# Kernel optimization log

Measured on AMD Instinct MI355X. Metric: run time of the kernel, lower is better.

## Reference

```python
import jax, jax.numpy as jnp
import numpy as np

N = 50000          # nodes
E = 800000         # edges (before self-loops)
F_IN, F_HID, F_OUT = 128, 64, 64
NEG_SLOPE_ATT = 0.2   # GATConv internal leaky_relu
NEG_SLOPE_ACT = 0.01  # F.leaky_relu default between layers


def setup_inputs() -> dict:
    key = jax.random.key(0)
    ks = jax.random.split(key, 16)

    def glorot(k, shape):
        fan = float(sum(shape)) if len(shape) > 1 else float(shape[0])
        return jax.random.normal(k, shape, jnp.float32) * (2.0 / fan) ** 0.5

    return {
        "x": jax.random.normal(ks[0], (N, F_IN), jnp.float32),
        "edge_index": jax.random.randint(ks[1], (2, E), 0, N, dtype=jnp.int64),
        "W1": glorot(ks[2], (F_IN, F_HID)),
        "a_src1": glorot(ks[3], (F_HID,)),
        "a_dst1": glorot(ks[4], (F_HID,)),
        "b1": jnp.zeros((F_HID,), jnp.float32),
        "W2": glorot(ks[5], (F_HID, F_HID)),
        "a_src2": glorot(ks[6], (F_HID,)),
        "a_dst2": glorot(ks[7], (F_HID,)),
        "b2": jnp.zeros((F_HID,), jnp.float32),
        "W3": glorot(ks[8], (F_HID, F_OUT)),
        "a_src3": glorot(ks[9], (F_OUT,)),
        "a_dst3": glorot(ks[10], (F_OUT,)),
        "b3": jnp.zeros((F_OUT,), jnp.float32),
    }


def gat_conv(h, src, dst, W, a_src, a_dst, b):
    # Single-head PyG GATConv: project, per-edge scores, segment softmax over dst, scatter-add.
    z = h @ W                              # [N, C]
    e_src = z @ a_src                      # [N]
    e_dst = z @ a_dst                      # [N]
    e = jax.nn.leaky_relu(e_src[src] + e_dst[dst], NEG_SLOPE_ATT)  # [E']
    m = jax.ops.segment_max(e, dst, num_segments=N)
    ex = jnp.exp(e - m[dst])
    denom = jax.ops.segment_sum(ex, dst, num_segments=N)
    alpha = ex / (denom[dst] + 1e-16)      # segment softmax (PyG adds 1e-16)
    out = jax.ops.segment_sum(alpha[:, None] * z[src], dst, num_segments=N) + b
    return out, alpha


def reference(x, edge_index, W1, a_src1, a_dst1, b1, W2, a_src2, a_dst2, b2, W3, a_src3, a_dst3, b3):
    # add_self_loops=True (GATConv default): append (i, i) for every node
    loops = jnp.arange(N, dtype=edge_index.dtype)
    ei = jnp.concatenate([edge_index, jnp.stack([loops, loops])], axis=1)  # [2, E+N]
    src, dst = ei[0], ei[1]

    h = x
    alpha = None
    for (W, asr, ads, b) in ((W1, a_src1, a_dst1, b1),
                             (W2, a_src2, a_dst2, b2),
                             (W3, a_src3, a_dst3, b3)):
        h, alpha = gat_conv(h, src, dst, W, asr, ads, b)
        h = jax.nn.leaky_relu(h, NEG_SLOPE_ACT)
    return (h, ei, alpha)
```

## Files before the change

### kernel.cpp

```cpp
#include <hip/hip_runtime.h>
#include <hip/hip_bf16.h>
#include <hip/hip_fp8.h>

#define NN 50000
#define EE 800000
#define E2 850000
#define F_IN 128
#define F_HID 64
#define NCHUNK ((NN + 255) / 256)
#define NTILE  ((NN + 63) / 64)
#define AGGB 2048

#define PNB 32
#define BCAP 32768
#define CBCH 512
#define CBB ((EE + CBCH - 1) / CBCH)
#define CBCAP 48
#define SLICEB 64

__device__ __forceinline__ unsigned char f32_to_fp8(float x) {
    __hip_fp8_e4m3 t(x);
    return t.__x;
}
__device__ __forceinline__ float fp8_to_f32(unsigned char b) {
    __hip_fp8_e4m3 t; t.__x = b;
    return (float)t;
}

#if defined(__has_builtin)
#  if __has_builtin(__builtin_amdgcn_cvt_f32_fp8)
#    define CVT_FP8(v, s) __builtin_amdgcn_cvt_f32_fp8((v), (s))
#  endif
#endif
#ifndef CVT_FP8
#  define CVT_FP8(v, s) fp8_to_f32(((v) >> (8 * (s))) & 255)
#endif

__global__ __launch_bounds__(256) void cast_bin_kernel(const int* __restrict__ ei,
                                                       int* __restrict__ bin_cur,
                                                       unsigned long long* __restrict__ bins,
                                                       float* __restrict__ ei_out) {
    __shared__ unsigned long long buf[PNB * CBCAP];
    __shared__ int cnt[PNB];
    __shared__ int gbase[PNB];
    __shared__ int pfx[PNB + 1];
    int tid = threadIdx.x;
    if (tid < PNB) cnt[tid] = 0;
    __syncthreads();

    int e0 = blockIdx.x * CBCH;
    int e1 = e0 + CBCH; if (e1 > EE) e1 = EE;
    for (int e = e0 + tid; e < e1; e += 256) {
        int s = ei[e], d = ei[EE + e];
        ei_out[e]      = (float)s;
        ei_out[E2 + e] = (float)d;
        int b = (int)(((long long)d * PNB) / NN);
        unsigned long long pk = ((unsigned long long)(unsigned)d << 32) | (unsigned)s;
        int r = atomicAdd(&cnt[b], 1);
        if (r < CBCAP) buf[b * CBCAP + r] = pk;
        else {
            int p = atomicAdd(&bin_cur[b], 1);
            if (p < BCAP) bins[(size_t)b * BCAP + p] = pk;
        }
    }
    __syncthreads();
    if (tid < PNB) {
        int c = cnt[tid]; if (c > CBCAP) c = CBCAP;
        cnt[tid] = c;
        gbase[tid] = c ? atomicAdd(&bin_cur[tid], c) : 0;
    }
    __syncthreads();
    if (tid == 0) {
        int run = 0;
        for (int b = 0; b < PNB; ++b) { pfx[b] = run; run += cnt[b]; }
        pfx[PNB] = run;
    }
    __syncthreads();
    int total = pfx[PNB];
    for (int idx = tid; idx < total; idx += 256) {
        int lo = 0, hi = PNB;
        while (hi - lo > 1) { int mid = (lo + hi) >> 1; if (pfx[mid] <= idx) lo = mid; else hi = mid; }
        int b = lo, li = idx - pfx[b];
        int p = gbase[b] + li;
        if (p < BCAP) bins[(size_t)b * BCAP + p] = buf[b * CBCAP + li];
    }
}

__global__ __launch_bounds__(256) void count_bins(const int* __restrict__ bin_cur,
                                                  const unsigned long long* __restrict__ bins,
                                                  int* __restrict__ deg) {
    int b = blockIdx.x & (PNB - 1);
    int slice = blockIdx.x >> 5;
    int cnt = bin_cur[b];
    if (cnt > BCAP) cnt = BCAP;
    const unsigned long long* bp = bins + (size_t)b * BCAP;
    for (int i = slice * 256 + threadIdx.x; i < cnt; i += SLICEB * 256) {
        int d = (int)(bp[i] >> 32);
        atomicAdd(&deg[d], 1);
    }
}

__global__ __launch_bounds__(256) void scan_part12(const int* __restrict__ deg,
                                                   int* __restrict__ csum,
                                                   int* __restrict__ ticket) {
    int i = blockIdx.x * 256 + threadIdx.x;
    int v = (i < NN) ? deg[i] + 1 : 0;
#pragma unroll
    for (int d = 32; d; d >>= 1) v += __shfl_xor(v, d);
    __shared__ int ws[4];
    if ((threadIdx.x & 63) == 0) ws[threadIdx.x >> 6] = v;
    __syncthreads();
    __shared__ int isLast;
    if (threadIdx.x == 0) {
        atomicExch(&csum[blockIdx.x], ws[0] + ws[1] + ws[2] + ws[3]);
        __threadfence();
        isLast = (atomicAdd(ticket, 1) == gridDim.x - 1) ? 1 : 0;
    }
    __syncthreads();
    if (isLast) {
        __threadfence();
        __shared__ int sd[256];
        int t = threadIdx.x;
        int v2 = (t < NCHUNK) ? atomicAdd(&csum[t], 0) : 0;
        sd[t] = v2;
        __syncthreads();
        for (int off = 1; off < 256; off <<= 1) {
            int o = (t >= off) ? sd[t - off] : 0;
            __syncthreads();
            sd[t] += o;
            __syncthreads();
        }
        if (t < NCHUNK) atomicExch(&csum[t], sd[t] - v2);
    }
}

__global__ __launch_bounds__(256) void scan_part3(const int* __restrict__ deg,
                                                  const int* __restrict__ csum,
                                                  int* __restrict__ offs,
                                                  int* __restrict__ cursor,
                                                  int* __restrict__ src_sorted,
                                                  float* __restrict__ ei_out) {
    __shared__ int sd[256];
    int t = threadIdx.x;
    int i = blockIdx.x * 256 + t;
    int v = (i < NN) ? deg[i] + 1 : 0;
    sd[t] = v;
    __syncthreads();
    for (int off = 1; off < 256; off <<= 1) {
        int o = (t >= off) ? sd[t - off] : 0;
        __syncthreads();
        sd[t] += o;
        __syncthreads();
    }
    if (i < NN) {
        int ex = sd[t] - v + csum[blockIdx.x];
        offs[i] = ex;
        cursor[i] = ex + 1;
        src_sorted[ex] = i;
        ei_out[EE + i]      = (float)i;
        ei_out[E2 + EE + i] = (float)i;
    }
}

__global__ __launch_bounds__(256) void scatter_bins(const int* __restrict__ bin_cur,
                                                    const unsigned long long* __restrict__ bins,
                                                    int* __restrict__ cursor,
                                                    int* __restrict__ src_sorted) {
    int b = blockIdx.x & (PNB - 1);
    int slice = blockIdx.x >> 5;
    int cnt = bin_cur[b];
    if (cnt > BCAP) cnt = BCAP;
    const unsigned long long* bp = bins + (size_t)b * BCAP;
    for (int i = slice * 256 + threadIdx.x; i < cnt; i += SLICEB * 256) {
        unsigned long long v = bp[i];
        int d = (int)(v >> 32);
        int s = (int)(v & 0xffffffffu);
        int pos = atomicAdd(&cursor[d], 1);
        src_sorted[pos] = s;
    }
}

template <int K>
__global__ __launch_bounds__(256) void gemm_tile(const float* __restrict__ h,
                                                 const float* __restrict__ W,
                                                 const float* __restrict__ a_src,
                                                 const float* __restrict__ a_dst,
                                                 unsigned char* __restrict__ z8,
                                                 float* __restrict__ es,
                                                 float* __restrict__ ed) {
    constexpr int LDA = K + 4;
    __shared__ float Alds[64 * LDA];
    __shared__ float Blds[K * 64];

    int tid = threadIdx.x;
    int base = blockIdx.x * 64;

    {
        constexpr int F4R = K / 4;
        for (int t = tid; t < 64 * F4R; t += 256) {
            int r = t / F4R;
            int c4 = t % F4R;
            int gr = base + r;
            if (gr >= NN) gr = NN - 1;
            float4 v = *(const float4*)(h + (size_t)gr * K + c4 * 4);
            *(float4*)(&Alds[r * LDA + c4 * 4]) = v;
        }
    }
    for (int t = tid; t < K * 16; t += 256) {
        float4 v = *(const float4*)(W + t * 4);
        *(float4*)(&Blds[t * 4]) = v;
    }
    __syncthreads();

    int tx = tid & 15;
    int ty = tid >> 4;

    float acc[4][4] = {};
#pragma unroll 4
    for (int k = 0; k < K; k += 4) {
        float4 a[4], b[4];
#pragma unroll
        for (int i = 0; i < 4; ++i)
            a[i] = *(const float4*)(&Alds[(4 * ty + i) * LDA + k]);
#pragma unroll
        for (int kk = 0; kk < 4; ++kk)
            b[kk] = *(const float4*)(&Blds[(k + kk) * 64 + 4 * tx]);
#pragma unroll
        for (int i = 0; i < 4; ++i) {
            acc[i][0] = fmaf(a[i].x, b[0].x, acc[i][0]);
            acc[i][1] = fmaf(a[i].x, b[0].y, acc[i][1]);
            acc[i][2] = fmaf(a[i].x, b[0].z, acc[i][2]);
            acc[i][3] = fmaf(a[i].x, b[0].w, acc[i][3]);
            acc[i][0] = fmaf(a[i].y, b[1].x, acc[i][0]);
            acc[i][1] = fmaf(a[i].y, b[1].y, acc[i][1]);
            acc[i][2] = fmaf(a[i].y, b[1].z, acc[i][2]);
            acc[i][3] = fmaf(a[i].y, b[1].w, acc[i][3]);
            acc[i][0] = fmaf(a[i].z, b[2].x, acc[i][0]);
            acc[i][1] = fmaf(a[i].z, b[2].y, acc[i][1]);
            acc[i][2] = fmaf(a[i].z, b[2].z, acc[i][2]);
            acc[i][3] = fmaf(a[i].z, b[2].w, acc[i][3]);
            acc[i][0] = fmaf(a[i].w, b[3].x, acc[i][0]);
            acc[i][1] = fmaf(a[i].w, b[3].y, acc[i][1]);
            acc[i][2] = fmaf(a[i].w, b[3].z, acc[i][2]);
            acc[i][3] = fmaf(a[i].w, b[3].w, acc[i][3]);
        }
    }

    float4 as4 = *(const float4*)(a_src + 4 * tx);
    float4 ad4 = *(const float4*)(a_dst + 4 * tx);
    float ps[4], pd[4];
#pragma unroll
    for (int i = 0; i < 4; ++i) {
        int gr = base + 4 * ty + i;
        if (gr < NN) {
            unsigned int pk = (unsigned int)f32_to_fp8(acc[i][0])
                            | ((unsigned int)f32_to_fp8(acc[i][1]) << 8)
                            | ((unsigned int)f32_to_fp8(acc[i][2]) << 16)
                            | ((unsigned int)f32_to_fp8(acc[i][3]) << 24);
            *(unsigned int*)(&z8[(size_t)gr * 64 + 4 * tx]) = pk;
        }
        ps[i] = acc[i][0] * as4.x + acc[i][1] * as4.y + acc[i][2] * as4.z + acc[i][3] * as4.w;
        pd[i] = acc[i][0] * ad4.x + acc[i][1] * ad4.y + acc[i][2] * ad4.z + acc[i][3] * ad4.w;
    }
#pragma unroll
    for (int d = 1; d < 16; d <<= 1) {
#pragma unroll
        for (int i = 0; i < 4; ++i) {
            ps[i] += __shfl_xor(ps[i], d);
            pd[i] += __shfl_xor(pd[i], d);
        }
    }
    if (tx == 0) {
#pragma unroll
        for (int i = 0; i < 4; ++i) {
            int gr = base + 4 * ty + i;
            if (gr < NN) { es[gr] = ps[i]; ed[gr] = pd[i]; }
        }
    }
}

__global__ __launch_bounds__(256) void aggregate(const int* __restrict__ offs,
                                                 const int* __restrict__ deg,
                                                 const int* __restrict__ src_sorted,
                                                 const float* __restrict__ es,
                                                 const float* __restrict__ ed,
                                                 const unsigned char* __restrict__ z8,
                                                 const float* __restrict__ bias,
                                                 float* __restrict__ hout,
                                                 float* __restrict__ denom_out) {
    int tid = threadIdx.x;
    int lane = tid & 63;
    int wave = blockIdx.x * 4 + (tid >> 6);
    const int NW = AGGB * 4;

    int sub  = lane >> 4;
    int fgrp = (lane & 15) * 4;
    const unsigned char* zp = z8 + fgrp;
    float4 bi4 = *(const float4*)(bias + fgrp);

    int n = wave;
    if (n >= NN) return;
    n = __builtin_amdgcn_readfirstlane(n);
    int off = offs[n];
    int dg = deg[n] + 1;
    float edn = ed[n];
    int sv = src_sorted[off + ((lane < dg) ? lane : 0)];
    float ese = es[sv];

    while (true) {
        int n2 = n + NW;
        bool more = (n2 < NN);
        int off2 = 0, dg2 = 0; float edn2 = 0.f;
        if (more) {
            n2 = __builtin_amdgcn_readfirstlane(n2);
            off2 = offs[n2]; dg2 = deg[n2] + 1; edn2 = ed[n2];
        }

        float dsum = 0.f;
        float a0 = 0.f, a1 = 0.f, a2 = 0.f, a3 = 0.f;
        for (int b0 = 0; b0 < dg; b0 += 64) {
            int bl = dg - b0; if (bl > 64) bl = 64;
            int svb; float esv;
            if (b0 == 0) { svb = sv; esv = ese; }
            else {
                svb = src_sorted[off + b0 + ((lane < bl) ? lane : 0)];
                esv = es[svb];
            }
            float e = esv + edn;
            e = (e > 0.f) ? e : 0.2f * e;
            float w = (lane < bl) ? __expf(e) : 0.f;
            dsum += w;

            int ng = (bl + 3) >> 2;
            int j = 0;
            for (; j + 4 <= ng; j += 4) {
                int i0 = 4 * j + sub;
                int   s0 = __shfl(svb, i0);
                int   s1 = __shfl(svb, i0 + 4);
                int   s2 = __shfl(svb, i0 + 8);
                int   s3 = __shfl(svb, i0 + 12);
                unsigned int v0 = *(const unsigned int*)(zp + (size_t)s0 * 64);
                unsigned int v1 = *(const unsigned int*)(zp + (size_t)s1 * 64);
                unsigned int v2 = *(const unsigned int*)(zp + (size_t)s2 * 64);
                unsigned int v3 = *(const unsigned int*)(zp + (size_t)s3 * 64);
                float w0 = __shfl(w, i0);
                float w1 = __shfl(w, i0 + 4);
                float w2 = __shfl(w, i0 + 8);
                float w3 = __shfl(w, i0 + 12);
                a0 = fmaf(w0, CVT_FP8(v0, 0), a0);
                a1 = fmaf(w0, CVT_FP8(v0, 1), a1);
                a2 = fmaf(w0, CVT_FP8(v0, 2), a2);
                a3 = fmaf(w0, CVT_FP8(v0, 3), a3);
                a0 = fmaf(w1, CVT_FP8(v1, 0), a0);
                a1 = fmaf(w1, CVT_FP8(v1, 1), a1);
                a2 = fmaf(w1, CVT_FP8(v1, 2), a2);
                a3 = fmaf(w1, CVT_FP8(v1, 3), a3);
                a0 = fmaf(w2, CVT_FP8(v2, 0), a0);
                a1 = fmaf(w2, CVT_FP8(v2, 1), a1);
                a2 = fmaf(w2, CVT_FP8(v2, 2), a2);
                a3 = fmaf(w2, CVT_FP8(v2, 3), a3);
                a0 = fmaf(w3, CVT_FP8(v3, 0), a0);
                a1 = fmaf(w3, CVT_FP8(v3, 1), a1);
                a2 = fmaf(w3, CVT_FP8(v3, 2), a2);
                a3 = fmaf(w3, CVT_FP8(v3, 3), a3);
            }
            for (; j < ng; ++j) {
                int i0 = 4 * j + sub;
                int   s0 = __shfl(svb, i0);
                unsigned int v0 = *(const unsigned int*)(zp + (size_t)s0 * 64);
                float w0 = __shfl(w, i0);
                a0 = fmaf(w0, CVT_FP8(v0, 0), a0);
                a1 = fmaf(w0, CVT_FP8(v0, 1), a1);
                a2 = fmaf(w0, CVT_FP8(v0, 2), a2);
                a3 = fmaf(w0, CVT_FP8(v0, 3), a3);
            }
        }

        int sv2 = 0;
        if (more) sv2 = src_sorted[off2 + ((lane < dg2) ? lane : 0)];

        a0 += __shfl_xor(a0, 16); a1 += __shfl_xor(a1, 16);
        a2 += __shfl_xor(a2, 16); a3 += __shfl_xor(a3, 16);
        a0 += __shfl_xor(a0, 32); a1 += __shfl_xor(a1, 32);
        a2 += __shfl_xor(a2, 32); a3 += __shfl_xor(a3, 32);
#pragma unroll
        for (int d = 32; d; d >>= 1) dsum += __shfl_xor(dsum, d);

        float ese2 = 0.f;
        if (more) ese2 = es[sv2];

        float inv = 1.f / (dsum + 1e-16f);
        if (lane < 16) {
            float4 o;
            o.x = a0 * inv + bi4.x;
            o.y = a1 * inv + bi4.y;
            o.z = a2 * inv + bi4.z;
            o.w = a3 * inv + bi4.w;
            o.x = (o.x > 0.f) ? o.x : 0.01f * o.x;
            o.y = (o.y > 0.f) ? o.y : 0.01f * o.y;
            o.z = (o.z > 0.f) ? o.z : 0.01f * o.z;
            o.w = (o.w > 0.f) ? o.w : 0.01f * o.w;
            *(float4*)(hout + (size_t)n * 64 + fgrp) = o;
        }
        if (lane == 0) denom_out[n] = dsum;

        if (!more) break;
        n = n2; off = off2; dg = dg2; edn = edn2; sv = sv2; ese = ese2;
    }
}

__global__ __launch_bounds__(256) void alpha_kernel(const int* __restrict__ ei,
                                                    const float* __restrict__ es,
                                                    const float* __restrict__ ed,
                                                    const float* __restrict__ denom,
                                                    float* __restrict__ alpha_out) {
    int e = blockIdx.x * 256 + threadIdx.x;
    if (e >= E2) return;
    int s, d;
    if (e < EE) { s = ei[e]; d = ei[EE + e]; }
    else        { s = d = e - EE; }
    float x = es[s] + ed[d];
    x = (x > 0.f) ? x : 0.2f * x;
    alpha_out[e] = __expf(x) / (denom[d] + 1e-16f);
}

extern "C" void kernel_launch(void* const* d_in, const int* in_sizes, int n_in,
                              void* d_out, int out_size, void* d_ws, size_t ws_size,
                              hipStream_t stream) {
    const float* x   = (const float*)d_in[0];
    const int*   ei  = (const int*)d_in[1];
    const float* W1  = (const float*)d_in[2];
    const float* as1 = (const float*)d_in[3];
    const float* ad1 = (const float*)d_in[4];
    const float* b1  = (const float*)d_in[5];
    const float* W2  = (const float*)d_in[6];
    const float* as2 = (const float*)d_in[7];
    const float* ad2 = (const float*)d_in[8];
    const float* b2  = (const float*)d_in[9];
    const float* W3  = (const float*)d_in[10];
    const float* as3 = (const float*)d_in[11];
    const float* ad3 = (const float*)d_in[12];
    const float* b3  = (const float*)d_in[13];

    float* out       = (float*)d_out;
    float* h_out     = out;
    float* ei_out    = out + (size_t)NN * 64;
    float* alpha_out = ei_out + 2 * (size_t)E2;

    char* w = (char*)d_ws;
    auto carve = [&](size_t bytes) {
        void* p = (void*)w;
        w += (bytes + 255) & ~size_t(255);
        return p;
    };
    float* h1  = (float*)carve((size_t)NN * 64 * 4);
    float* h2  = (float*)carve((size_t)NN * 64 * 4);
    unsigned char* z8 = (unsigned char*)carve((size_t)NN * 64);
    float* es  = (float*)carve((size_t)NN * 4);
    float* ed  = (float*)carve((size_t)NN * 4);
    float* denom = (float*)carve((size_t)NN * 4);
    int* deg        = (int*)carve(((size_t)NN + 64) * 4);
    int* ticket     = deg + NN;
    int* bin_cur    = deg + NN + 1;
    int* offs       = (int*)carve((size_t)NN * 4);
    int* cursor     = (int*)carve((size_t)NN * 4);
    int* csum       = (int*)carve((size_t)NCHUNK * 4);
    int* src_sorted = (int*)carve((size_t)E2 * 4);
    unsigned long long* bins = (unsigned long long*)carve((size_t)PNB * BCAP * 8);

    const int EB = (E2 + 255) / 256;

    hipMemsetAsync(deg, 0, ((size_t)NN + 64) * 4, stream);
    cast_bin_kernel<<<CBB, 256, 0, stream>>>(ei, bin_cur, bins, ei_out);
    count_bins<<<PNB * SLICEB, 256, 0, stream>>>(bin_cur, bins, deg);
    scan_part12<<<NCHUNK, 256, 0, stream>>>(deg, csum, ticket);
    scan_part3<<<NCHUNK, 256, 0, stream>>>(deg, csum, offs, cursor, src_sorted, ei_out);
    scatter_bins<<<PNB * SLICEB, 256, 0, stream>>>(bin_cur, bins, cursor, src_sorted);

    gemm_tile<F_IN><<<NTILE, 256, 0, stream>>>(x, W1, as1, ad1, z8, es, ed);
    aggregate<<<AGGB, 256, 0, stream>>>(offs, deg, src_sorted, es, ed, z8, b1, h1, denom);
    gemm_tile<F_HID><<<NTILE, 256, 0, stream>>>(h1, W2, as2, ad2, z8, es, ed);
    aggregate<<<AGGB, 256, 0, stream>>>(offs, deg, src_sorted, es, ed, z8, b2, h2, denom);
    gemm_tile<F_HID><<<NTILE, 256, 0, stream>>>(h2, W3, as3, ad3, z8, es, ed);
    aggregate<<<AGGB, 256, 0, stream>>>(offs, deg, src_sorted, es, ed, z8, b3, h_out, denom);
    alpha_kernel<<<EB, 256, 0, stream>>>(ei, es, ed, denom, alpha_out);
}
```

Measured before the change: 315.6 us.

## Fuse degree histogram into binning kernel and stage edge weights in LDS

Merges the separate degree-counting pass into the edge binning kernel, so degrees are counted with global atomics while edges are read, and drops one launch plus a re-read of the bins. Binning now processes 1024 edges per block and ranks edges within each wave using ballots instead of per-edge shared atomics. The aggregate kernel writes packed (weight, source offset) pairs into LDS and reads them back, replacing the per-edge shuffles of source index and weight. The costs are a 32-iteration ballot loop per edge batch and extra LDS traffic.

Result: faster. 307.1 us (-2.7%).

```diff
diff --git a/kernel.cpp b/kernel.cpp
--- a/kernel.cpp
+++ b/kernel.cpp
@@ -13,9 +13,9 @@
 
 #define PNB 32
 #define BCAP 32768
-#define CBCH 512
-#define CBB ((EE + CBCH - 1) / CBCH)
-#define CBCAP 48
+#define HBCH 1024
+#define HBB ((EE + HBCH - 1) / HBCH)
+#define HCAP 64
 #define SLICEB 64
 
 __device__ __forceinline__ unsigned char f32_to_fp8(float x) {
@@ -36,67 +36,93 @@
 #  define CVT_FP8(v, s) fp8_to_f32(((v) >> (8 * (s))) & 255)
 #endif
 
-__global__ __launch_bounds__(256) void cast_bin_kernel(const int* __restrict__ ei,
-                                                       int* __restrict__ bin_cur,
-                                                       unsigned long long* __restrict__ bins,
-                                                       float* __restrict__ ei_out) {
-    __shared__ unsigned long long buf[PNB * CBCAP];
-    __shared__ int cnt[PNB];
+__global__ __launch_bounds__(256) void hist_bin2(const int* __restrict__ ei,
+                                                 int* __restrict__ deg,
+                                                 int* __restrict__ bin_cur,
+                                                 unsigned long long* __restrict__ bins,
+                                                 float* __restrict__ ei_out) {
+    __shared__ unsigned long long buf[PNB * HCAP];
+    __shared__ int wcnt[4][PNB];
+    __shared__ int woff[4][PNB];
+    __shared__ int tcn[PNB];
     __shared__ int gbase[PNB];
     __shared__ int pfx[PNB + 1];
-    int tid = threadIdx.x;
-    if (tid < PNB) cnt[tid] = 0;
-    __syncthreads();
-
-    int e0 = blockIdx.x * CBCH;
-    int e1 = e0 + CBCH; if (e1 > EE) e1 = EE;
-    for (int e = e0 + tid; e < e1; e += 256) {
-        int s = ei[e], d = ei[EE + e];
-        ei_out[e]      = (float)s;
-        ei_out[E2 + e] = (float)d;
-        int b = (int)(((long long)d * PNB) / NN);
-        unsigned long long pk = ((unsigned long long)(unsigned)d << 32) | (unsigned)s;
-        int r = atomicAdd(&cnt[b], 1);
-        if (r < CBCAP) buf[b * CBCAP + r] = pk;
-        else {
-            int p = atomicAdd(&bin_cur[b], 1);
-            if (p < BCAP) bins[(size_t)b * BCAP + p] = pk;
-        }
-    }
-    __syncthreads();
+
+    int tid = threadIdx.x, lane = tid & 63, wv = tid >> 6;
+    if (tid < 4 * PNB) ((int*)wcnt)[tid] = 0;
+    __syncthreads();
+
+    int e0 = blockIdx.x * HBCH;
+    int nE = EE - e0; if (nE > HBCH) nE = HBCH;
+
+    int sR[4], dR[4], bR[4], rk[4];
+    bool act[4];
+#pragma unroll
+    for (int it = 0; it < 4; ++it) {
+        int idx = it * 256 + tid;
+        bool a = idx < nE;
+        act[it] = a;
+        int e = e0 + idx;
+        int ss = 0, dd = 0;
+        if (a) { ss = ei[e]; dd = ei[EE + e]; }
+        if (a) {
+            atomicAdd(&deg[dd], 1);
+            ei_out[e]      = (float)ss;
+            ei_out[E2 + e] = (float)dd;
+        }
+        int bb = a ? (int)(((long long)dd * PNB) / NN) : -1;
+        int myrank = 0;
+        for (int bin = 0; bin < PNB; ++bin) {
+            unsigned long long m = __ballot(bb == bin);
+            if (bb == bin) {
+                int base = wcnt[wv][bin];
+                int lr = __popcll(m & ((1ull << lane) - 1));
+                myrank = base + lr;
+                if (lr == 0) wcnt[wv][bin] = base + __popcll(m);
+            }
+        }
+        sR[it] = ss; dR[it] = dd; bR[it] = bb; rk[it] = myrank;
+    }
+    __syncthreads();
+
     if (tid < PNB) {
-        int c = cnt[tid]; if (c > CBCAP) c = CBCAP;
-        cnt[tid] = c;
-        gbase[tid] = c ? atomicAdd(&bin_cur[tid], c) : 0;
+        int b = tid, r = 0;
+        for (int w2 = 0; w2 < 4; ++w2) { int c = wcnt[w2][b]; woff[w2][b] = r; r += c; }
+        int cl = (r > HCAP) ? HCAP : r;
+        tcn[b] = cl;
+        gbase[b] = cl ? atomicAdd(&bin_cur[b], cl) : 0;
     }
     __syncthreads();
     if (tid == 0) {
         int run = 0;
-        for (int b = 0; b < PNB; ++b) { pfx[b] = run; run += cnt[b]; }
+        for (int b = 0; b < PNB; ++b) { pfx[b] = run; run += tcn[b]; }
         pfx[PNB] = run;
     }
     __syncthreads();
+
+#pragma unroll
+    for (int it = 0; it < 4; ++it) {
+        if (act[it]) {
+            int b = bR[it];
+            int idx = woff[wv][b] + rk[it];
+            unsigned long long pk =
+                ((unsigned long long)(unsigned)dR[it] << 32) | (unsigned)sR[it];
+            if (idx < HCAP) buf[b * HCAP + idx] = pk;
+            else {
+                int p = atomicAdd(&bin_cur[b], 1);
+                if (p < BCAP) bins[(size_t)b * BCAP + p] = pk;
+            }
+        }
+    }
+    __syncthreads();
+
     int total = pfx[PNB];
     for (int idx = tid; idx < total; idx += 256) {
         int lo = 0, hi = PNB;
         while (hi - lo > 1) { int mid = (lo + hi) >> 1; if (pfx[mid] <= idx) lo = mid; else hi = mid; }
         int b = lo, li = idx - pfx[b];
         int p = gbase[b] + li;
-        if (p < BCAP) bins[(size_t)b * BCAP + p] = buf[b * CBCAP + li];
-    }
-}
-
-__global__ __launch_bounds__(256) void count_bins(const int* __restrict__ bin_cur,
-                                                  const unsigned long long* __restrict__ bins,
-                                                  int* __restrict__ deg) {
-    int b = blockIdx.x & (PNB - 1);
-    int slice = blockIdx.x >> 5;
-    int cnt = bin_cur[b];
-    if (cnt > BCAP) cnt = BCAP;
-    const unsigned long long* bp = bins + (size_t)b * BCAP;
-    for (int i = slice * 256 + threadIdx.x; i < cnt; i += SLICEB * 256) {
-        int d = (int)(bp[i] >> 32);
-        atomicAdd(&deg[d], 1);
+        if (p < BCAP) bins[(size_t)b * BCAP + p] = buf[b * HCAP + li];
     }
 }
 
@@ -288,9 +314,11 @@
                                                  const float* __restrict__ bias,
                                                  float* __restrict__ hout,
                                                  float* __restrict__ denom_out) {
+    __shared__ unsigned long long swl[4][64];
     int tid = threadIdx.x;
     int lane = tid & 63;
-    int wave = blockIdx.x * 4 + (tid >> 6);
+    int wslot = tid >> 6;
+    int wave = blockIdx.x * 4 + wslot;
     const int NW = AGGB * 4;
 
     int sub  = lane >> 4;
@@ -331,22 +359,25 @@
             float w = (lane < bl) ? __expf(e) : 0.f;
             dsum += w;
 
+            swl[wslot][lane] = ((unsigned long long)__float_as_uint(w) << 32)
+                             | (unsigned)(svb << 6);
+
             int ng = (bl + 3) >> 2;
             int j = 0;
             for (; j + 4 <= ng; j += 4) {
                 int i0 = 4 * j + sub;
-                int   s0 = __shfl(svb, i0);
-                int   s1 = __shfl(svb, i0 + 4);
-                int   s2 = __shfl(svb, i0 + 8);
-                int   s3 = __shfl(svb, i0 + 12);
-                unsigned int v0 = *(const unsigned int*)(zp + (size_t)s0 * 64);
-                unsigned int v1 = *(const unsigned int*)(zp + (size_t)s1 * 64);
-                unsigned int v2 = *(const unsigned int*)(zp + (size_t)s2 * 64);
-                unsigned int v3 = *(const unsigned int*)(zp + (size_t)s3 * 64);
-                float w0 = __shfl(w, i0);
-                float w1 = __shfl(w, i0 + 4);
-                float w2 = __shfl(w, i0 + 8);
-                float w3 = __shfl(w, i0 + 12);
+                unsigned long long p0 = swl[wslot][i0];
+                unsigned long long p1 = swl[wslot][i0 + 4];
+                unsigned long long p2 = swl[wslot][i0 + 8];
+                unsigned long long p3 = swl[wslot][i0 + 12];
+                unsigned int v0 = *(const unsigned int*)(zp + (unsigned)p0);
+                unsigned int v1 = *(const unsigned int*)(zp + (unsigned)p1);
+                unsigned int v2 = *(const unsigned int*)(zp + (unsigned)p2);
+                unsigned int v3 = *(const unsigned int*)(zp + (unsigned)p3);
+                float w0 = __uint_as_float((unsigned)(p0 >> 32));
+                float w1 = __uint_as_float((unsigned)(p1 >> 32));
+                float w2 = __uint_as_float((unsigned)(p2 >> 32));
+                float w3 = __uint_as_float((unsigned)(p3 >> 32));
                 a0 = fmaf(w0, CVT_FP8(v0, 0), a0);
                 a1 = fmaf(w0, CVT_FP8(v0, 1), a1);
                 a2 = fmaf(w0, CVT_FP8(v0, 2), a2);
@@ -366,9 +397,9 @@
             }
             for (; j < ng; ++j) {
                 int i0 = 4 * j + sub;
-                int   s0 = __shfl(svb, i0);
-                unsigned int v0 = *(const unsigned int*)(zp + (size_t)s0 * 64);
-                float w0 = __shfl(w, i0);
+                unsigned long long p0 = swl[wslot][i0];
+                unsigned int v0 = *(const unsigned int*)(zp + (unsigned)p0);
+                float w0 = __uint_as_float((unsigned)(p0 >> 32));
                 a0 = fmaf(w0, CVT_FP8(v0, 0), a0);
                 a1 = fmaf(w0, CVT_FP8(v0, 1), a1);
                 a2 = fmaf(w0, CVT_FP8(v0, 2), a2);
@@ -471,8 +502,7 @@
     const int EB = (E2 + 255) / 256;
 
     hipMemsetAsync(deg, 0, ((size_t)NN + 64) * 4, stream);
-    cast_bin_kernel<<<CBB, 256, 0, stream>>>(ei, bin_cur, bins, ei_out);
-    count_bins<<<PNB * SLICEB, 256, 0, stream>>>(bin_cur, bins, deg);
+    hist_bin2<<<HBB, 256, 0, stream>>>(ei, deg, bin_cur, bins, ei_out);
     scan_part12<<<NCHUNK, 256, 0, stream>>>(deg, csum, ticket);
     scan_part3<<<NCHUNK, 256, 0, stream>>>(deg, csum, offs, cursor, src_sorted, ei_out);
     scatter_bins<<<PNB * SLICEB, 256, 0, stream>>>(bin_cur, bins, cursor, src_sorted);
```
